# Optimization experiments

Measured on AMD Instinct MI355X. Metric: run time of the kernel, lower is better.

The kernel has to match this reference:

```python
import jax, jax.numpy as jnp
import numpy as np

NEG_INF_CONST = -2.0**32 + 1.0  # matches torch module's self.inf


def setup_inputs() -> dict:
    key = jax.random.key(0)
    kq, kk, kv = jax.random.split(key, 3)
    B, L, S, H, E, D = 2, 2048, 2048, 8, 64, 64
    return {
        "queries": jax.random.normal(kq, (B, L, H, E), dtype=jnp.float32),
        "keys": jax.random.normal(kk, (B, S, H, E), dtype=jnp.float32),
        "values": jax.random.normal(kv, (B, S, H, D), dtype=jnp.float32),
    }


def reference(queries, keys, values):
    B, L, H, E = queries.shape
    _, S, _, D = values.shape
    scale = 1.0 / np.sqrt(E).astype(np.float32)
    # Faithful to torch: .view(B*H, L, E) on a contiguous [B, L, H, E] tensor
    # reinterprets memory row-major (mixes L and H), same as jnp.reshape.
    q = queries.reshape(B * H, L, E)
    k = keys.reshape(B * H, S, E)
    # squared pairwise L2 distance == cdist(...).pow(2)
    d2 = (
        jnp.sum(q * q, axis=-1)[:, :, None]
        + jnp.sum(k * k, axis=-1)[:, None, :]
        - 2.0 * jnp.einsum("nle,nse->nls", q, k)
    )
    d2 = jnp.maximum(d2, 0.0).reshape(B, H, L, S)
    scores = 1.0 - jnp.exp(-d2)  # dropout is identity in eval mode
    causal = jnp.tril(jnp.ones((L, S), dtype=bool))  # mask.tril(diagonal=0)
    scores = jnp.where(causal, scores, jnp.float32(NEG_INF_CONST))
    A = jax.nn.softmax(scale * scores, axis=-1)
    return jnp.einsum("bhls,bshd->blhd", A, values)
```

## Files before the change

kernel.cpp:

```cpp
#include <hip/hip_runtime.h>
#include <hip/hip_bf16.h>

typedef __attribute__((ext_vector_type(8))) __bf16 bf16x8;
typedef __attribute__((ext_vector_type(4))) float f32x4;

namespace {

constexpr int L = 2048;
constexpr int E = 64;
constexpr int NHEAD = 16;
constexpr float SCALE = 0.125f;
constexpr float LOG2E = 1.44269504f;
constexpr float TWO_LOG2E = 2.88539008f;

constexpr size_t KN_OFF = 4096;
constexpr size_t KB_OFF = KN_OFF + (size_t)NHEAD * L * 4;
constexpr size_t VT_OFF = KB_OFF + (size_t)NHEAD * L * E * 2;

__device__ __forceinline__ int swz(int row, int byte_in_row) {
  const int f = (row & 3) | (((row >> 3) & 1) << 2);
  return row * 128 + (byte_in_row ^ (f << 4));
}

__device__ __forceinline__ unsigned pack_bf16(float a, float b) {
  union { __bf16 h[2]; unsigned u; } p;
  p.h[0] = (__bf16)a; p.h[1] = (__bf16)b;
  return p.u;
}

__device__ __forceinline__ void cvt_row16(const float4* src, float& pn,
                                          bf16x8& w0, bf16x8& w1) {
  float4 a = src[0], c = src[1];
  pn += a.x*a.x + a.y*a.y + a.z*a.z + a.w*a.w;
  pn += c.x*c.x + c.y*c.y + c.z*c.z + c.w*c.w;
  w0[0]=(__bf16)a.x; w0[1]=(__bf16)a.y; w0[2]=(__bf16)a.z; w0[3]=(__bf16)a.w;
  w0[4]=(__bf16)c.x; w0[5]=(__bf16)c.y; w0[6]=(__bf16)c.z; w0[7]=(__bf16)c.w;
  float4 d = src[2], e = src[3];
  pn += d.x*d.x + d.y*d.y + d.z*d.z + d.w*d.w;
  pn += e.x*e.x + e.y*e.y + e.z*e.z + e.w*e.w;
  w1[0]=(__bf16)d.x; w1[1]=(__bf16)d.y; w1[2]=(__bf16)d.z; w1[3]=(__bf16)d.w;
  w1[4]=(__bf16)e.x; w1[5]=(__bf16)e.y; w1[6]=(__bf16)e.z; w1[7]=(__bf16)e.w;
}

__global__ __launch_bounds__(256)
void prep(const float* __restrict__ Kg, const float* __restrict__ Vg,
          __bf16* __restrict__ Kb, float* __restrict__ kn,
          __bf16* __restrict__ Vt) {
  __shared__ float Vs[64][65];
  const int t = threadIdx.x;
  if (blockIdx.x < 512) {
    const int row = blockIdx.x * 64 + (t >> 2);
    const int seg = t & 3;
    const float4* src = reinterpret_cast<const float4*>(
        Kg + (size_t)row * E + seg * 16);
    float pn = 0.f; bf16x8 w0, w1;
    cvt_row16(src, pn, w0, w1);
    __bf16* dst = Kb + (size_t)row * E + seg * 16;
    *reinterpret_cast<bf16x8*>(dst)     = w0;
    *reinterpret_cast<bf16x8*>(dst + 8) = w1;
    pn += __shfl_xor(pn, 1);
    pn += __shfl_xor(pn, 2);
    if (seg == 0) kn[row] = -LOG2E * pn;
  } else {
    const int bb = blockIdx.x - 512;
    const int n  = bb >> 5;
    const int st = bb & 31;
    const int b = n >> 3, h = n & 7;
    {
      const int srow = t >> 2, seg = t & 3;
      const float4* src = reinterpret_cast<const float4*>(
          Vg + ((size_t)b * L + st * 64 + srow) * 512 + h * 64 + seg * 16);
      #pragma unroll
      for (int jj = 0; jj < 4; ++jj) {
        float4 a = src[jj];
        Vs[srow][seg*16 + jj*4 + 0] = a.x;
        Vs[srow][seg*16 + jj*4 + 1] = a.y;
        Vs[srow][seg*16 + jj*4 + 2] = a.z;
        Vs[srow][seg*16 + jj*4 + 3] = a.w;
      }
    }
    __syncthreads();
    {
      const int d = t >> 2, sg = t & 3;
      bf16x8 o0, o1;
      #pragma unroll
      for (int i = 0; i < 8; ++i) o0[i] = (__bf16)Vs[sg*16 + i][d];
      #pragma unroll
      for (int i = 0; i < 8; ++i) o1[i] = (__bf16)Vs[sg*16 + 8 + i][d];
      __bf16* dst = Vt + (size_t)n * (E * L) + (size_t)d * L + st * 64 + sg * 16;
      *reinterpret_cast<bf16x8*>(dst)     = o0;
      *reinterpret_cast<bf16x8*>(dst + 8) = o1;
    }
  }
}

__global__ __launch_bounds__(512, 4)
void degr_attn(const float* __restrict__ Qg, const __bf16* __restrict__ Kb,
               const __bf16* __restrict__ Vt, const float* __restrict__ kng,
               float* __restrict__ Og) {
  __shared__ char smem[65536];

  const int id = blockIdx.x;
  const int n  = (id & 7) | (((id >> 3) & 1) << 3);
  const int u  = id >> 4;
  const int lt = 31 - u;
  const int l0 = lt * 64;
  const int b = n >> 3, h = n & 7;

  const int t = threadIdx.x;
  const int wave = t >> 6, grp = wave >> 2, w4 = wave & 3;
  const int lane = t & 63, lg = lane >> 4, lr = lane & 15;
  const int gt = t & 255;

  char* kbase = smem + grp * 32768;
  char* vbase = smem + grp * 32768 + 16384;
  float*  Cbuf = (float*)smem;
  float*  Dbuf = (float*)(smem + 17408);

  const float*  Qh  = Qg  + (size_t)n * (L * E);
  const __bf16* Kh  = Kb  + (size_t)n * (L * E);
  const __bf16* Vh  = Vt  + (size_t)n * (E * L);
  const float*  knh = kng + (size_t)n * L;

  const int l_glob = l0 + 16 * w4 + lr;
  bf16x8 qf0, qf1;
  float qnL;
  {
    const float* qp = Qh + (size_t)l_glob * E + 8 * lg;
    float4 a = *reinterpret_cast<const float4*>(qp);
    float4 d = *reinterpret_cast<const float4*>(qp + 4);
    float4 a2 = *reinterpret_cast<const float4*>(qp + 32);
    float4 d2v = *reinterpret_cast<const float4*>(qp + 36);
    float pn = 0.f;
    #pragma unroll
    for (int i = 0; i < 4; ++i) {
      float v0 = (i==0)?a.x:(i==1)?a.y:(i==2)?a.z:a.w;
      float v1 = (i==0)?d.x:(i==1)?d.y:(i==2)?d.z:d.w;
      float v2 = (i==0)?a2.x:(i==1)?a2.y:(i==2)?a2.z:a2.w;
      float v3 = (i==0)?d2v.x:(i==1)?d2v.y:(i==2)?d2v.z:d2v.w;
      qf0[i]   = (__bf16)v0;  qf0[i+4] = (__bf16)v1;
      qf1[i]   = (__bf16)v2;  qf1[i+4] = (__bf16)v3;
      float f;
      f = (float)qf0[i];   pn += f*f;
      f = (float)qf0[i+4]; pn += f*f;
      f = (float)qf1[i];   pn += f*f;
      f = (float)qf1[i+4]; pn += f*f;
    }
    pn += __shfl_xor(pn, 16);
    pn += __shfl_xor(pn, 32);
    qnL = -LOG2E * pn;
  }

  const int srow = gt >> 2;
  const int scol = (gt & 3) * 2;
  const int wk0 = swz(srow, scol*16);
  const int wk1 = swz(srow, scol*16 + 16);
  int koffL[4], koffH[4];
  #pragma unroll
  for (int hx = 0; hx < 4; ++hx) {
    const int krow = 32*(hx>>1) + 8*(lr>>2) + 4*(hx&1) + (lr&3);
    koffL[hx] = swz(krow, lg*16);
    koffH[hx] = swz(krow, 64 + lg*16);
  }
  int voff[2][4];
  #pragma unroll
  for (int sc = 0; sc < 2; ++sc)
    #pragma unroll
    for (int dsb = 0; dsb < 4; ++dsb)
      voff[sc][dsb] = swz(dsb*16 + lr, sc*64 + lg*16);

  bf16x8 kr0, kr1, vr0, vr1;
  auto loadKV = [&](int c) {
    const int s0 = c * 64;
    const __bf16* kp = Kh + (size_t)(s0 + srow) * E + scol * 8;
    kr0 = *reinterpret_cast<const bf16x8*>(kp);
    kr1 = *reinterpret_cast<const bf16x8*>(kp + 8);
    const __bf16* vp = Vh + (size_t)srow * L + s0 + scol * 8;
    vr0 = *reinterpret_cast<const bf16x8*>(vp);
    vr1 = *reinterpret_cast<const bf16x8*>(vp + 8);
  };
  auto writeKV = [&](int WB) {
    *reinterpret_cast<bf16x8*>(kbase + WB + wk0) = kr0;
    *reinterpret_cast<bf16x8*>(kbase + WB + wk1) = kr1;
    *reinterpret_cast<bf16x8*>(vbase + WB + wk0) = vr0;
    *reinterpret_cast<bf16x8*>(vbase + WB + wk1) = vr1;
  };

  const int n_it = (lt >> 1) + 1;
  loadKV(grp <= lt ? grp : lt);
  writeKV(0);
  __syncthreads();

  f32x4 oacc[4];
  #pragma unroll
  for (int i = 0; i < 4; ++i) oacc[i] = (f32x4){0.f, 0.f, 0.f, 0.f};
  float den = 0.f;

  auto body = [&](int i, const int B, const bool MASK) {
    const int c = 2 * i + grp;
    const bool more = (i + 1 < n_it);
    if (more) {
      int cn = 2 * (i + 1) + grp;
      loadKV(cn <= lt ? cn : lt);
    }
    const int s_base = c * 64;
    const char* kb = kbase + B;
    const char* vb = vbase + B;

    float4 kn4[4];
    kn4[0] = *reinterpret_cast<const float4*>(knh + s_base + 8*lg);
    kn4[1] = *reinterpret_cast<const float4*>(knh + s_base + 8*lg + 4);
    kn4[2] = *reinterpret_cast<const float4*>(knh + s_base + 32 + 8*lg);
    kn4[3] = *reinterpret_cast<const float4*>(knh + s_base + 36 + 8*lg);

    __builtin_amdgcn_s_setprio(1);
    unsigned up[4][2];
    #pragma unroll
    for (int hx = 0; hx < 4; ++hx) {
      const bf16x8 kf0 = *reinterpret_cast<const bf16x8*>(kb + koffL[hx]);
      const bf16x8 kf1 = *reinterpret_cast<const bf16x8*>(kb + koffH[hx]);
      f32x4 acc = (f32x4){0.f, 0.f, 0.f, 0.f};
      acc = __builtin_amdgcn_mfma_f32_16x16x32_bf16(kf0, qf0, acc, 0, 0, 0);
      acc = __builtin_amdgcn_mfma_f32_16x16x32_bf16(kf1, qf1, acc, 0, 0, 0);
      float w[4];
      #pragma unroll
      for (int r = 0; r < 4; ++r) {
        const float knv = (r==0)?kn4[hx].x:(r==1)?kn4[hx].y:(r==2)?kn4[hx].z:kn4[hx].w;
        float arg = fminf(fmaf(TWO_LOG2E, acc[r], qnL + knv), 0.f);
        float e1  = __builtin_amdgcn_exp2f(arg);
        float y   = fmaf(-SCALE, e1, SCALE);
        float tt  = fmaf(0.5f, y, 1.0f);
        float wv  = fmaf(y, tt, 1.0f);
        if (MASK) {
          const int sof = 32*(hx>>1) + 8*lg + 4*(hx&1);
          wv = (s_base + sof + r <= l_glob) ? wv : 0.f;
        }
        den += wv;
        w[r] = wv;
      }
      up[hx][0] = pack_bf16(w[0], w[1]);
      up[hx][1] = pack_bf16(w[2], w[3]);
    }
    #pragma unroll
    for (int sc = 0; sc < 2; ++sc) {
      union { unsigned u[4]; bf16x8 v; } pb;
      pb.u[0] = up[2*sc][0];
      pb.u[1] = up[2*sc][1];
      pb.u[2] = up[2*sc+1][0];
      pb.u[3] = up[2*sc+1][1];
      const bf16x8 pf = pb.v;
      #pragma unroll
      for (int dsb = 0; dsb < 4; ++dsb) {
        const bf16x8 vf = *reinterpret_cast<const bf16x8*>(vb + voff[sc][dsb]);
        oacc[dsb] = __builtin_amdgcn_mfma_f32_16x16x32_bf16(pf, vf, oacc[dsb], 0, 0, 0);
      }
    }
    __builtin_amdgcn_s_setprio(0);

    if (more) writeKV(B ^ 8192);
    __syncthreads();
  };

  {
    int i = 0;
    for (; i + 2 < n_it; i += 2) { body(i, 0, false); body(i + 1, 8192, false); }
    if ((n_it & 1) == 0) { body(n_it - 2, 0, false); body(n_it - 1, 8192, true); }
    else                 { body(n_it - 1, 0, true); }
  }

  den += __shfl_xor(den, 16);
  den += __shfl_xor(den, 32);

  if (grp == 1) {
    #pragma unroll
    for (int dsb = 0; dsb < 4; ++dsb)
      #pragma unroll
      for (int r = 0; r < 4; ++r)
        Cbuf[(16*w4 + 4*lg + r) * 65 + 16*dsb + lr] = oacc[dsb][r];
    if (lane < 16) Dbuf[16*w4 + lr] = den;
  }
  __syncthreads();
  if (grp == 0) {
    const float dtot = den + Dbuf[16*w4 + lr];
    float inv[4];
    #pragma unroll
    for (int r = 0; r < 4; ++r)
      inv[r] = 1.0f / __shfl(dtot, 4*lg + r);
    float* obase = Og + ((size_t)b * L + l0 + 16*w4) * 512 + h * 64;
    #pragma unroll
    for (int r = 0; r < 4; ++r) {
      float* orow = obase + (size_t)(4*lg + r) * 512;
      #pragma unroll
      for (int dsb = 0; dsb < 4; ++dsb) {
        const float s = oacc[dsb][r] + Cbuf[(16*w4 + 4*lg + r) * 65 + 16*dsb + lr];
        orow[16*dsb + lr] = s * inv[r];
      }
    }
  }
}

}

extern "C" void kernel_launch(void* const* d_in, const int* in_sizes, int n_in,
                              void* d_out, int out_size, void* d_ws, size_t ws_size,
                              hipStream_t stream) {
  (void)in_sizes; (void)n_in; (void)out_size; (void)ws_size;
  const float* q = (const float*)d_in[0];
  const float* k = (const float*)d_in[1];
  const float* v = (const float*)d_in[2];
  float*       o = (float*)d_out;

  char* ws = (char*)d_ws;
  float*  kn = (float*)(ws + KN_OFF);
  __bf16* Kb = (__bf16*)(ws + KB_OFF);
  __bf16* Vt = (__bf16*)(ws + VT_OFF);

  prep<<<dim3(1024), dim3(256), 0, stream>>>(k, v, Kb, kn, Vt);
  degr_attn<<<dim3(512), dim3(512), 0, stream>>>(q, Kb, Vt, kn, o);
}
```

Measured before the change: 40.16 us.

## Single-buffer K/V tiles in LDS and zigzag tile order for load balance

Halves the LDS footprint by dropping the double-buffered K/V staging. Each iteration now computes from one buffer, syncs, writes the prefetched tile, and syncs again. This is meant to let more blocks share a CU. The block-to-query-tile mapping changes from longest-first to a zigzag order so short and long causal tiles pair up. Chunks past the diagonal are now skipped instead of computed fully masked. The cost is an extra barrier per iteration and less overlap between LDS writes and compute.

```diff
diff --git a/kernel.cpp b/kernel.cpp
--- a/kernel.cpp
+++ b/kernel.cpp
@@ -98,12 +98,12 @@
 void degr_attn(const float* __restrict__ Qg, const __bf16* __restrict__ Kb,
                const __bf16* __restrict__ Vt, const float* __restrict__ kng,
                float* __restrict__ Og) {
-  __shared__ char smem[65536];
+  __shared__ char smem[32768];
 
   const int id = blockIdx.x;
   const int n  = (id & 7) | (((id >> 3) & 1) << 3);
   const int u  = id >> 4;
-  const int lt = 31 - u;
+  const int lt = (u < 16) ? u : 47 - u;
   const int l0 = lt * 64;
   const int b = n >> 3, h = n & 7;
 
@@ -112,8 +112,8 @@
   const int lane = t & 63, lg = lane >> 4, lr = lane & 15;
   const int gt = t & 255;
 
-  char* kbase = smem + grp * 32768;
-  char* vbase = smem + grp * 32768 + 16384;
+  char* kbase = smem + grp * 16384;
+  char* vbase = kbase + 8192;
   float*  Cbuf = (float*)smem;
   float*  Dbuf = (float*)(smem + 17408);
 
@@ -179,34 +179,20 @@
     vr0 = *reinterpret_cast<const bf16x8*>(vp);
     vr1 = *reinterpret_cast<const bf16x8*>(vp + 8);
   };
-  auto writeKV = [&](int WB) {
-    *reinterpret_cast<bf16x8*>(kbase + WB + wk0) = kr0;
-    *reinterpret_cast<bf16x8*>(kbase + WB + wk1) = kr1;
-    *reinterpret_cast<bf16x8*>(vbase + WB + wk0) = vr0;
-    *reinterpret_cast<bf16x8*>(vbase + WB + wk1) = vr1;
+  auto writeKV = [&]() {
+    *reinterpret_cast<bf16x8*>(kbase + wk0) = kr0;
+    *reinterpret_cast<bf16x8*>(kbase + wk1) = kr1;
+    *reinterpret_cast<bf16x8*>(vbase + wk0) = vr0;
+    *reinterpret_cast<bf16x8*>(vbase + wk1) = vr1;
   };
-
-  const int n_it = (lt >> 1) + 1;
-  loadKV(grp <= lt ? grp : lt);
-  writeKV(0);
-  __syncthreads();
 
   f32x4 oacc[4];
   #pragma unroll
   for (int i = 0; i < 4; ++i) oacc[i] = (f32x4){0.f, 0.f, 0.f, 0.f};
   float den = 0.f;
 
-  auto body = [&](int i, const int B, const bool MASK) {
-    const int c = 2 * i + grp;
-    const bool more = (i + 1 < n_it);
-    if (more) {
-      int cn = 2 * (i + 1) + grp;
-      loadKV(cn <= lt ? cn : lt);
-    }
+  auto compute = [&](int c, bool MASK) {
     const int s_base = c * 64;
-    const char* kb = kbase + B;
-    const char* vb = vbase + B;
-
     float4 kn4[4];
     kn4[0] = *reinterpret_cast<const float4*>(knh + s_base + 8*lg);
     kn4[1] = *reinterpret_cast<const float4*>(knh + s_base + 8*lg + 4);
@@ -217,8 +203,8 @@
     unsigned up[4][2];
     #pragma unroll
     for (int hx = 0; hx < 4; ++hx) {
-      const bf16x8 kf0 = *reinterpret_cast<const bf16x8*>(kb + koffL[hx]);
-      const bf16x8 kf1 = *reinterpret_cast<const bf16x8*>(kb + koffH[hx]);
+      const bf16x8 kf0 = *reinterpret_cast<const bf16x8*>(kbase + koffL[hx]);
+      const bf16x8 kf1 = *reinterpret_cast<const bf16x8*>(kbase + koffH[hx]);
       f32x4 acc = (f32x4){0.f, 0.f, 0.f, 0.f};
       acc = __builtin_amdgcn_mfma_f32_16x16x32_bf16(kf0, qf0, acc, 0, 0, 0);
       acc = __builtin_amdgcn_mfma_f32_16x16x32_bf16(kf1, qf1, acc, 0, 0, 0);
@@ -251,21 +237,30 @@
       const bf16x8 pf = pb.v;
       #pragma unroll
       for (int dsb = 0; dsb < 4; ++dsb) {
-        const bf16x8 vf = *reinterpret_cast<const bf16x8*>(vb + voff[sc][dsb]);
+        const bf16x8 vf = *reinterpret_cast<const bf16x8*>(vbase + voff[sc][dsb]);
         oacc[dsb] = __builtin_amdgcn_mfma_f32_16x16x32_bf16(pf, vf, oacc[dsb], 0, 0, 0);
       }
     }
     __builtin_amdgcn_s_setprio(0);
-
-    if (more) writeKV(B ^ 8192);
+  };
+
+  const int n_it = (lt >> 1) + 1;
+  loadKV(grp <= lt ? grp : lt);
+  writeKV();
+  __syncthreads();
+  for (int i = 0; i < n_it; ++i) {
+    const int c = 2 * i + grp;
+    const bool more = (i + 1 < n_it);
+    if (more) {
+      int cn = 2 * (i + 1) + grp;
+      loadKV(cn <= lt ? cn : lt);
+    }
+    if (c <= lt) compute(c, c == lt);
     __syncthreads();
-  };
-
-  {
-    int i = 0;
-    for (; i + 2 < n_it; i += 2) { body(i, 0, false); body(i + 1, 8192, false); }
-    if ((n_it & 1) == 0) { body(n_it - 2, 0, false); body(n_it - 1, 8192, true); }
-    else                 { body(n_it - 1, 0, true); }
+    if (more) {
+      writeKV();
+      __syncthreads();
+    }
   }
 
   den += __shfl_xor(den, 16);
```

After: 45.49 us. 1.13x slower.
